# Performance work log

Hardware: AMD Instinct MI355X
Metric: run time of the kernel (lower is better)

Reference implementation:

```python
import jax, jax.numpy as jnp
import numpy as np

N_NODES = 100000
N_EDGES = 1600000
D = 128  # node_feat_size == edge_hidden_size


def setup_inputs() -> dict:
    key = jax.random.key(0)
    ks = jax.random.split(key, 10)
    s = 1.0 / np.sqrt(D)
    return {
        "node_feats": jax.random.normal(ks[0], (N_NODES, D), jnp.float32),
        "edge_logits": jax.random.normal(ks[1], (N_EDGES, 1), jnp.float32),
        "W_proj": jax.random.normal(ks[2], (D, D), jnp.float32) * s,
        "b_proj": jax.random.normal(ks[3], (D,), jnp.float32) * s,
        "W1": jax.random.normal(ks[4], (2 * D, D), jnp.float32) * s,
        "b1": jax.random.normal(ks[5], (D,), jnp.float32) * s,
        "W2": jax.random.normal(ks[6], (D, D), jnp.float32) * s,
        "b2": jax.random.normal(ks[7], (D,), jnp.float32) * s,
        "src": jax.random.randint(ks[8], (N_EDGES,), 0, N_NODES),
        "dst": jax.random.randint(ks[9], (N_EDGES,), 0, N_NODES),
    }


def reference(node_feats, edge_logits, W_proj, b_proj, W1, b1, W2, b2, src, dst):
    # ---- edge_softmax: softmax of edge_logits grouped by destination node ----
    # [E,1] logits; per-dst max for numerical stability (gradient-free shift)
    m = jax.ops.segment_max(edge_logits, dst, num_segments=N_NODES)  # [N,1]
    m = jnp.where(jnp.isfinite(m), m, 0.0)  # nodes with no in-edges
    e = jnp.exp(edge_logits - jax.lax.stop_gradient(m)[dst])  # [E,1]
    z = jax.ops.segment_sum(e, dst, num_segments=N_NODES)  # [N,1]
    a = e / z[dst]  # [E,1]

    # ---- project_node (dropout is identity at inference) ----
    hv = node_feats @ W_proj + b_proj  # [N,D]

    # ---- src_mul_edge + sum aggregation: c[v] = sum_{(u->v)} a_uv * hv[u] ----
    msg = hv[src] * a  # [E,D]
    c = jax.ops.segment_sum(msg, dst, num_segments=N_NODES)  # [N,D]

    context = jax.nn.elu(c)
    x = jnp.concatenate([context, node_feats], axis=1)  # [N,2D]
    h = jax.nn.relu(x @ W1 + b1)  # Linear -> Dropout(id) -> ReLU
    out = jax.nn.relu(h @ W2 + b2)  # Linear -> Dropout(id), outer ReLU
    return out
```

## Files before the change

### kernel.cpp

```cpp
#include <hip/hip_runtime.h>
#include <hip/hip_bf16.h>

typedef __hip_bfloat16 bf16;
typedef __attribute__((ext_vector_type(8))) __bf16 bf16x8;
typedef __attribute__((ext_vector_type(4))) float floatx4;
typedef __attribute__((ext_vector_type(2))) float floatx2;

#define BUCKET_SHIFT 7
#define BUCKET_NODES 128
#define MAX_NB 1024
#define EPB 2048

__device__ __forceinline__ unsigned short f2b(float f) {
    bf16 h = __float2bfloat16(f);
    unsigned short s;
    __builtin_memcpy(&s, &h, 2);
    return s;
}
__device__ __forceinline__ float b2f(unsigned short u) {
    unsigned int x = ((unsigned int)u) << 16;
    float f;
    __builtin_memcpy(&f, &x, 4);
    return f;
}
__device__ __forceinline__ float load_dual(const void* p, long long i, bool isbf) {
    return isbf ? b2f(((const unsigned short*)p)[i]) : ((const float*)p)[i];
}
__device__ __forceinline__ bf16x8 ldsfrag(const unsigned short* p) {
    union { uint4 u; bf16x8 v; } t;
    t.u = *(const uint4*)p;
    return t.v;
}
__device__ __forceinline__ bf16x8 gfrag_dual(const void* A, int row, int stride, int k0, bool isbf) {
    if (isbf) {
        union { uint4 u; bf16x8 v; } t;
        t.u = *(const uint4*)((const unsigned short*)A + (size_t)row * stride + k0);
        return t.v;
    }
    const float* ap = (const float*)A + (size_t)row * stride + k0;
    float4 v0 = ((const float4*)ap)[0];
    float4 v1 = ((const float4*)ap)[1];
    union { unsigned short s[8]; bf16x8 v; } t;
    t.s[0] = f2b(v0.x); t.s[1] = f2b(v0.y); t.s[2] = f2b(v0.z); t.s[3] = f2b(v0.w);
    t.s[4] = f2b(v1.x); t.s[5] = f2b(v1.y); t.s[6] = f2b(v1.z); t.s[7] = f2b(v1.w);
    return t.v;
}

__global__ __launch_bounds__(64) void detect_kernel(const unsigned int* __restrict__ words,
                                                    int* __restrict__ flag,
                                                    int* __restrict__ bcount) {
    for (int i = threadIdx.x; i < MAX_NB; i += 64) bcount[i] = 0;
    int cnt = 0;
    for (int i = threadIdx.x; i < 4096; i += 64) {
        unsigned int lo = words[i] & 0xFFFFu;
        unsigned int e = (lo >> 7) & 0xFFu;
        if (lo == 0u || (e >= 110u && e <= 135u)) cnt++;
    }
#pragma unroll
    for (int off = 32; off > 0; off >>= 1) cnt += __shfl_down(cnt, off, 64);
    if (threadIdx.x == 0) *flag = (cnt > 2458) ? 1 : 0;
}

__global__ __launch_bounds__(256) void prep_kernel(const void* __restrict__ Wp,
                                                   const void* __restrict__ W1,
                                                   const void* __restrict__ W2,
                                                   unsigned short* __restrict__ Wtp,
                                                   unsigned short* __restrict__ Wt1,
                                                   unsigned short* __restrict__ Wt2,
                                                   const int* __restrict__ flag,
                                                   const int* __restrict__ dst,
                                                   int* __restrict__ bcount, int E) {
    if (blockIdx.x < 256) {
        bool isbf = (*flag != 0);
        int idx = blockIdx.x * 256 + threadIdx.x;
        if (idx < 16384) {
            int n = idx >> 7, k = idx & 127;
            Wtp[idx] = f2b(load_dual(Wp, (long long)k * 128 + n, isbf));
        } else if (idx < 49152) {
            int j = idx - 16384;
            int n = j >> 8, k = j & 255;
            Wt1[j] = f2b(load_dual(W1, (long long)k * 128 + n, isbf));
        } else if (idx < 65536) {
            int j = idx - 49152;
            int n = j >> 7, k = j & 127;
            Wt2[j] = f2b(load_dual(W2, (long long)k * 128 + n, isbf));
        }
    } else {
        __shared__ int lcnt[MAX_NB];
        for (int i = threadIdx.x; i < MAX_NB; i += 256) lcnt[i] = 0;
        __syncthreads();
        int base = (blockIdx.x - 256) * EPB;
#pragma unroll
        for (int j = 0; j < EPB / 256; ++j) {
            int e = base + j * 256 + threadIdx.x;
            if (e < E) atomicAdd(&lcnt[dst[e] >> BUCKET_SHIFT], 1);
        }
        __syncthreads();
        for (int i = threadIdx.x; i < MAX_NB; i += 256)
            if (lcnt[i]) atomicAdd(&bcount[i], lcnt[i]);
    }
}

__global__ __launch_bounds__(256) void bscan_kernel(const int* __restrict__ bcount,
                                                    int* __restrict__ bstart,
                                                    int* __restrict__ bcursor, int NB) {
    int t = threadIdx.x;
    int v[4];
    int sum = 0;
#pragma unroll
    for (int j = 0; j < 4; ++j) {
        int i = t * 4 + j;
        v[j] = (i < NB) ? bcount[i] : 0;
        sum += v[j];
    }
    int lane = t & 63, wave = t >> 6;
    int inc = sum;
#pragma unroll
    for (int off = 1; off < 64; off <<= 1) {
        int x = __shfl_up(inc, off, 64);
        if (lane >= off) inc += x;
    }
    __shared__ int wsum[4];
    if (lane == 63) wsum[wave] = inc;
    __syncthreads();
    int woff = 0;
    for (int w = 0; w < wave; ++w) woff += wsum[w];
    int run = inc - sum + woff;
#pragma unroll
    for (int j = 0; j < 4; ++j) {
        int i = t * 4 + j;
        if (i < NB) { bstart[i] = run; bcursor[i] = run; }
        run += v[j];
    }
}

__global__ __launch_bounds__(256) void bappend_kernel(const int* __restrict__ dst,
                                                      const int* __restrict__ src,
                                                      const void* __restrict__ logits,
                                                      int* __restrict__ bcursor,
                                                      uint2* __restrict__ ebuf,
                                                      const int* __restrict__ flag, int E) {
    __shared__ int lcnt[MAX_NB];
    __shared__ int lbase[MAX_NB];
    for (int i = threadIdx.x; i < MAX_NB; i += 256) lcnt[i] = 0;
    __syncthreads();
    const bool isbf = (*flag != 0);
    int base = blockIdx.x * EPB;
#pragma unroll
    for (int j = 0; j < EPB / 256; ++j) {
        int e = base + j * 256 + threadIdx.x;
        if (e < E) atomicAdd(&lcnt[dst[e] >> BUCKET_SHIFT], 1);
    }
    __syncthreads();
    for (int i = threadIdx.x; i < MAX_NB; i += 256) {
        int c = lcnt[i];
        if (c) { lbase[i] = atomicAdd(&bcursor[i], c); lcnt[i] = 0; }
    }
    __syncthreads();
#pragma unroll
    for (int j = 0; j < EPB / 256; ++j) {
        int e = base + j * 256 + threadIdx.x;
        if (e < E) {
            int d = dst[e];
            int b = d >> BUCKET_SHIFT;
            float w = expf(load_dual(logits, e, isbf));
            int pos = lbase[b] + atomicAdd(&lcnt[b], 1);
            uint2 rec;
            rec.x = (unsigned int)src[e] | ((unsigned int)(d & (BUCKET_NODES - 1)) << 24);
            rec.y = __float_as_uint(w);
            ebuf[pos] = rec;
        }
    }
}

__global__ __launch_bounds__(256) void gemm_bcsr_kernel(const void* __restrict__ A,
                                                        const unsigned short* __restrict__ Wt,
                                                        const void* __restrict__ bias,
                                                        unsigned short* __restrict__ hv,
                                                        const int* __restrict__ flag, int N,
                                                        int gblocks,
                                                        const uint2* __restrict__ ebuf,
                                                        const int* __restrict__ bstart,
                                                        const int* __restrict__ bcount,
                                                        uint2* __restrict__ ebuf2,
                                                        int* __restrict__ row_start,
                                                        int* __restrict__ ncount) {
    __shared__ unsigned short Wl[128 * 136];
    if ((int)blockIdx.x < gblocks) {
        const bool isbf = (*flag != 0);
        const int t = threadIdx.x, wid = t >> 6, lane = t & 63;
        const int m16 = lane & 15, quad = lane >> 4;
        const int row0 = blockIdx.x * 128;
        {
            int r = t >> 1, kh = (t & 1) * 64;
            const uint4* s = (const uint4*)(Wt + (size_t)r * 128 + kh);
            uint4* d = (uint4*)&Wl[r * 136 + kh];
#pragma unroll
            for (int q = 0; q < 8; ++q) d[q] = s[q];
        }
        __syncthreads();

        floatx4 acc[2][8];
#pragma unroll
        for (int i = 0; i < 2; ++i)
#pragma unroll
            for (int j = 0; j < 8; ++j) acc[i][j] = (floatx4){0.f, 0.f, 0.f, 0.f};

        int ra0 = row0 + wid * 32 + m16;      if (ra0 >= N) ra0 = N - 1;
        int ra1 = row0 + wid * 32 + 16 + m16; if (ra1 >= N) ra1 = N - 1;

#pragma unroll
        for (int c = 0; c < 4; ++c) {
            int k0 = c * 32 + quad * 8;
            bf16x8 a0 = gfrag_dual(A, ra0, 128, k0, isbf);
            bf16x8 a1 = gfrag_dual(A, ra1, 128, k0, isbf);
#pragma unroll
            for (int nt = 0; nt < 8; ++nt) {
                bf16x8 b = ldsfrag(&Wl[(nt * 16 + m16) * 136 + k0]);
                acc[0][nt] = __builtin_amdgcn_mfma_f32_16x16x32_bf16(a0, b, acc[0][nt], 0, 0, 0);
                acc[1][nt] = __builtin_amdgcn_mfma_f32_16x16x32_bf16(a1, b, acc[1][nt], 0, 0, 0);
            }
        }

#pragma unroll
        for (int mt = 0; mt < 2; ++mt) {
            int gr0 = row0 + wid * 32 + mt * 16 + quad * 4;
#pragma unroll
            for (int nt = 0; nt < 8; ++nt) {
                int col = nt * 16 + m16;
                float bb = load_dual(bias, col, isbf);
#pragma unroll
                for (int rg = 0; rg < 4; ++rg) {
                    int gr = gr0 + rg;
                    if (gr < N) hv[(size_t)gr * 128 + col] = f2b(acc[mt][nt][rg] + bb);
                }
            }
        }
    } else {
        int* lcnt = (int*)Wl;
        int* lbase = lcnt + BUCKET_NODES;
        const int b = blockIdx.x - gblocks;
        const int s0 = bstart[b];
        const int cnt = bcount[b];
        if (threadIdx.x < BUCKET_NODES) lcnt[threadIdx.x] = 0;
        __syncthreads();
        for (int i = threadIdx.x; i < cnt; i += 256)
            atomicAdd(&lcnt[ebuf[s0 + i].x >> 24], 1);
        __syncthreads();
        if (threadIdx.x < 64) {
            int lane = threadIdx.x;
            int carry = 0;
#pragma unroll
            for (int half = 0; half < 2; ++half) {
                int idx = half * 64 + lane;
                int v = lcnt[idx];
                int inc = v;
#pragma unroll
                for (int off = 1; off < 64; off <<= 1) {
                    int t = __shfl_up(inc, off, 64);
                    if (lane >= off) inc += t;
                }
                lbase[idx] = carry + inc - v;
                carry += __shfl(inc, 63, 64);
            }
        }
        __syncthreads();
        if (threadIdx.x < BUCKET_NODES) {
            int gn = b * BUCKET_NODES + threadIdx.x;
            if (gn < N) {
                row_start[gn] = s0 + lbase[threadIdx.x];
                ncount[gn] = lcnt[threadIdx.x];
            }
        }
        __syncthreads();
        if (threadIdx.x < BUCKET_NODES) lcnt[threadIdx.x] = 0;
        __syncthreads();
        for (int i = threadIdx.x; i < cnt; i += 256) {
            uint2 rec = ebuf[s0 + i];
            int dl = rec.x >> 24;
            int pos = lbase[dl] + atomicAdd(&lcnt[dl], 1);
            ebuf2[s0 + pos] = make_uint2(rec.x & 0xFFFFFFu, rec.y);
        }
    }
}

__global__ __launch_bounds__(256) void agg_csr_kernel(const int* __restrict__ row_start,
                                                      const int* __restrict__ ncount,
                                                      const unsigned long long* __restrict__ erec,
                                                      const unsigned int* __restrict__ hv32,
                                                      unsigned int* __restrict__ ctx32, int N) {
    int n = blockIdx.x * 4 + (threadIdx.x >> 6);
    int lane = threadIdx.x & 63;
    if (n >= N) return;
    int s0 = __builtin_amdgcn_readfirstlane(row_start[n]);
    int deg = __builtin_amdgcn_readfirstlane(ncount[n]);
    const unsigned long long* ep = erec + s0;
    const unsigned int lb = (unsigned int)lane << 2;
    floatx2 acc = {0.f, 0.f};
    float z = 0.f;
    int i = 0;
    for (; i + 16 <= deg; i += 16) {
        unsigned long long r[16];
        unsigned int h[16];
#pragma unroll
        for (int j = 0; j < 16; ++j) r[j] = ep[i + j];
#pragma unroll
        for (int j = 0; j < 16; ++j) {
            unsigned int sx = (unsigned int)r[j];
            __builtin_assume(sx < (1u << 24));
            h[j] = *(const unsigned int*)((const char*)hv32 + ((sx << 8) | lb));
        }
#pragma unroll
        for (int j = 0; j < 16; ++j) {
            float w = __uint_as_float((unsigned int)(r[j] >> 32));
            z += w;
            floatx2 hf = { __uint_as_float(h[j] << 16),
                           __uint_as_float(h[j] & 0xFFFF0000u) };
            acc += hf * w;
        }
    }
    for (; i + 4 <= deg; i += 4) {
        unsigned long long r[4];
        unsigned int h[4];
#pragma unroll
        for (int j = 0; j < 4; ++j) r[j] = ep[i + j];
#pragma unroll
        for (int j = 0; j < 4; ++j) {
            unsigned int sx = (unsigned int)r[j];
            __builtin_assume(sx < (1u << 24));
            h[j] = *(const unsigned int*)((const char*)hv32 + ((sx << 8) | lb));
        }
#pragma unroll
        for (int j = 0; j < 4; ++j) {
            float w = __uint_as_float((unsigned int)(r[j] >> 32));
            z += w;
            floatx2 hf = { __uint_as_float(h[j] << 16),
                           __uint_as_float(h[j] & 0xFFFF0000u) };
            acc += hf * w;
        }
    }
    for (; i < deg; ++i) {
        unsigned long long r = ep[i];
        unsigned int sx = (unsigned int)r;
        __builtin_assume(sx < (1u << 24));
        unsigned int h = *(const unsigned int*)((const char*)hv32 + ((sx << 8) | lb));
        float w = __uint_as_float((unsigned int)(r >> 32));
        z += w;
        floatx2 hf = { __uint_as_float(h << 16),
                       __uint_as_float(h & 0xFFFF0000u) };
        acc += hf * w;
    }
    float rz = (z > 0.f) ? 1.f / z : 0.f;
    float x = acc.x * rz, y = acc.y * rz;
    x = x > 0.f ? x : expm1f(x);
    y = y > 0.f ? y : expm1f(y);
    ctx32[(size_t)n * 64 + lane] = ((unsigned int)f2b(y) << 16) | f2b(x);
}

__global__ __launch_bounds__(256) void mlp_fused(const unsigned short* __restrict__ ctx,
                                                 const void* __restrict__ nf,
                                                 const unsigned short* __restrict__ Wt1,
                                                 const void* __restrict__ b1,
                                                 const unsigned short* __restrict__ Wt2,
                                                 const void* __restrict__ b2,
                                                 void* __restrict__ outp,
                                                 const int* __restrict__ flag, int N) {
    __shared__ unsigned short Wl[128 * 72];
    __shared__ unsigned short Hl[4][32 * 136];
    const bool isbf = (*flag != 0);
    const int t = threadIdx.x, wid = t >> 6, lane = t & 63;
    const int m16 = lane & 15, quad = lane >> 4;
    const int row0 = blockIdx.x * 128;

    floatx4 acc[2][8];
#pragma unroll
    for (int i = 0; i < 2; ++i)
#pragma unroll
        for (int j = 0; j < 8; ++j) acc[i][j] = (floatx4){0.f, 0.f, 0.f, 0.f};

    int ra0 = row0 + wid * 32 + m16;      if (ra0 >= N) ra0 = N - 1;
    int ra1 = row0 + wid * 32 + 16 + m16; if (ra1 >= N) ra1 = N - 1;

#pragma unroll
    for (int kc = 0; kc < 4; ++kc) {
        {
            int r = t >> 1, kh = (t & 1) * 32;
            const uint4* s = (const uint4*)(Wt1 + (size_t)r * 256 + kc * 64 + kh);
            uint4* d = (uint4*)&Wl[r * 72 + kh];
#pragma unroll
            for (int q = 0; q < 4; ++q) d[q] = s[q];
        }
        __syncthreads();
#pragma unroll
        for (int c = 0; c < 2; ++c) {
            int kl = c * 32 + quad * 8;
            int ka = kc * 64 + kl;
            bf16x8 a0, a1;
            if (ka < 128) {
                union { uint4 u; bf16x8 v; } t0, t1;
                t0.u = *(const uint4*)(ctx + (size_t)ra0 * 128 + ka);
                t1.u = *(const uint4*)(ctx + (size_t)ra1 * 128 + ka);
                a0 = t0.v; a1 = t1.v;
            } else {
                a0 = gfrag_dual(nf, ra0, 128, ka - 128, isbf);
                a1 = gfrag_dual(nf, ra1, 128, ka - 128, isbf);
            }
#pragma unroll
            for (int nt = 0; nt < 8; ++nt) {
                bf16x8 b = ldsfrag(&Wl[(nt * 16 + m16) * 72 + kl]);
                acc[0][nt] = __builtin_amdgcn_mfma_f32_16x16x32_bf16(a0, b, acc[0][nt], 0, 0, 0);
                acc[1][nt] = __builtin_amdgcn_mfma_f32_16x16x32_bf16(a1, b, acc[1][nt], 0, 0, 0);
            }
        }
        __syncthreads();
    }

#pragma unroll
    for (int nt = 0; nt < 8; ++nt) {
        int col = nt * 16 + m16;
        float bb = load_dual(b1, col, isbf);
#pragma unroll
        for (int mt = 0; mt < 2; ++mt) {
#pragma unroll
            for (int rg = 0; rg < 4; ++rg) {
                int lr = mt * 16 + quad * 4 + rg;
                float x = acc[mt][nt][rg] + bb;
                Hl[wid][lr * 136 + col] = f2b(x > 0.f ? x : 0.f);
            }
        }
    }

#pragma unroll
    for (int i = 0; i < 2; ++i)
#pragma unroll
        for (int j = 0; j < 8; ++j) acc[i][j] = (floatx4){0.f, 0.f, 0.f, 0.f};

#pragma unroll
    for (int kc = 0; kc < 2; ++kc) {
        {
            int r = t >> 1, kh = (t & 1) * 32;
            const uint4* s = (const uint4*)(Wt2 + (size_t)r * 128 + kc * 64 + kh);
            uint4* d = (uint4*)&Wl[r * 72 + kh];
#pragma unroll
            for (int q = 0; q < 4; ++q) d[q] = s[q];
        }
        __syncthreads();
#pragma unroll
        for (int c = 0; c < 2; ++c) {
            int kl = c * 32 + quad * 8;
            int ka = kc * 64 + kl;
            bf16x8 a0 = ldsfrag(&Hl[wid][m16 * 136 + ka]);
            bf16x8 a1 = ldsfrag(&Hl[wid][(16 + m16) * 136 + ka]);
#pragma unroll
            for (int nt = 0; nt < 8; ++nt) {
                bf16x8 b = ldsfrag(&Wl[(nt * 16 + m16) * 72 + kl]);
                acc[0][nt] = __builtin_amdgcn_mfma_f32_16x16x32_bf16(a0, b, acc[0][nt], 0, 0, 0);
                acc[1][nt] = __builtin_amdgcn_mfma_f32_16x16x32_bf16(a1, b, acc[1][nt], 0, 0, 0);
            }
        }
        __syncthreads();
    }

#pragma unroll
    for (int mt = 0; mt < 2; ++mt) {
        int gr0 = row0 + wid * 32 + mt * 16 + quad * 4;
#pragma unroll
        for (int nt = 0; nt < 8; ++nt) {
            int col = nt * 16 + m16;
            float bb = load_dual(b2, col, isbf);
#pragma unroll
            for (int rg = 0; rg < 4; ++rg) {
                int gr = gr0 + rg;
                if (gr < N) {
                    float x = acc[mt][nt][rg] + bb;
                    x = x > 0.f ? x : 0.f;
                    if (!isbf) ((float*)outp)[(size_t)gr * 128 + col] = x;
                    else       ((unsigned short*)outp)[(size_t)gr * 128 + col] = f2b(x);
                }
            }
        }
    }
}

extern "C" void kernel_launch(void* const* d_in, const int* in_sizes, int n_in,
                              void* d_out, int out_size, void* d_ws, size_t ws_size,
                              hipStream_t stream) {
    const void* node_feats  = d_in[0];
    const void* edge_logits = d_in[1];
    const void* W_proj      = d_in[2];
    const void* b_proj      = d_in[3];
    const void* W1          = d_in[4];
    const void* b1          = d_in[5];
    const void* W2          = d_in[6];
    const void* b2          = d_in[7];
    const int*  src         = (const int*)d_in[8];
    const int*  dst         = (const int*)d_in[9];

    const int N = in_sizes[0] / 128;
    const int E = in_sizes[8];
    const int NB = (N + BUCKET_NODES - 1) / BUCKET_NODES;

    char* ws = (char*)d_ws;
    size_t off = 0;
    unsigned short* hv  = (unsigned short*)(ws + off); off += (size_t)N * 256;
    unsigned short* ctx = (unsigned short*)(ws + off); off += (size_t)N * 256;
    uint2* ebuf  = (uint2*)(ws + off); off += (size_t)E * 8;
    uint2* ebuf2 = (uint2*)(ws + off); off += (size_t)E * 8;
    unsigned short* Wtp = (unsigned short*)(ws + off); off += 128 * 128 * 2;
    unsigned short* Wt1 = (unsigned short*)(ws + off); off += 128 * 256 * 2;
    unsigned short* Wt2 = (unsigned short*)(ws + off); off += 128 * 128 * 2;
    int* bcount    = (int*)(ws + off); off += MAX_NB * 4;
    int* bstart    = (int*)(ws + off); off += MAX_NB * 4;
    int* bcursor   = (int*)(ws + off); off += MAX_NB * 4;
    int* row_start = (int*)(ws + off); off += (size_t)N * 4;
    int* ncount    = (int*)(ws + off); off += (size_t)N * 4;
    int* flag      = (int*)(ws + off);

    const int gblocks = (N + 127) / 128;
    const int ebblocks = (E + EPB - 1) / EPB;

    detect_kernel<<<1, 64, 0, stream>>>((const unsigned int*)node_feats, flag, bcount);
    prep_kernel<<<256 + ebblocks, 256, 0, stream>>>(W_proj, W1, W2, Wtp, Wt1, Wt2,
                                                    flag, dst, bcount, E);
    bscan_kernel<<<1, 256, 0, stream>>>(bcount, bstart, bcursor, NB);
    bappend_kernel<<<ebblocks, 256, 0, stream>>>(dst, src, edge_logits, bcursor,
                                                 ebuf, flag, E);
    gemm_bcsr_kernel<<<gblocks + NB, 256, 0, stream>>>(node_feats, Wtp, b_proj, hv,
                                                       flag, N, gblocks,
                                                       ebuf, bstart, bcount, ebuf2,
                                                       row_start, ncount);
    agg_csr_kernel<<<(N + 3) / 4, 256, 0, stream>>>(row_start, ncount,
                                                    (const unsigned long long*)ebuf2,
                                                    (const unsigned int*)hv,
                                                    (unsigned int*)ctx, N);
    mlp_fused<<<gblocks, 256, 0, stream>>>(ctx, node_feats, Wt1, b1, Wt2, b2,
                                           d_out, flag, N);
}
```

Baseline: 344.6 us.

## Fuse bucket counting and append into one segment-local sort pass

Replaces the separate count and append passes over the edges with a single kernel. Each block of 2048 edges bucket-sorts its edges locally in shared memory, writes them back contiguously in its own segment, and records per-bucket offsets for that segment. The later bucket kernel then gathers each bucket's slices from every segment into shared memory before the per-node sort. This removes one full pass over dst, src and logits plus the global cursor atomics. In exchange the gather is serialized per thread with uneven slice sizes, and a bucket holding more than 4352 edges is silently truncated, which assumes a fairly uniform dst distribution.

After: 352.0 us. 2.1% more time.

```diff
diff --git a/kernel.cpp b/kernel.cpp
--- a/kernel.cpp
+++ b/kernel.cpp
@@ -61,18 +61,30 @@
     if (threadIdx.x == 0) *flag = (cnt > 2458) ? 1 : 0;
 }
 
-__global__ __launch_bounds__(256) void prep_kernel(const void* __restrict__ Wp,
-                                                   const void* __restrict__ W1,
-                                                   const void* __restrict__ W2,
-                                                   unsigned short* __restrict__ Wtp,
-                                                   unsigned short* __restrict__ Wt1,
-                                                   unsigned short* __restrict__ Wt2,
-                                                   const int* __restrict__ flag,
-                                                   const int* __restrict__ dst,
-                                                   int* __restrict__ bcount, int E) {
-    if (blockIdx.x < 256) {
-        bool isbf = (*flag != 0);
-        int idx = blockIdx.x * 256 + threadIdx.x;
+__global__ __launch_bounds__(256) void sortseg_kernel(const int* __restrict__ dst,
+                                                      const int* __restrict__ src,
+                                                      const void* __restrict__ logits,
+                                                      uint2* __restrict__ ebuf,
+                                                      int* __restrict__ offs,
+                                                      int* __restrict__ bcount,
+                                                      const void* __restrict__ Wp,
+                                                      const void* __restrict__ W1,
+                                                      const void* __restrict__ W2,
+                                                      unsigned short* __restrict__ Wtp,
+                                                      unsigned short* __restrict__ Wt1,
+                                                      unsigned short* __restrict__ Wt2,
+                                                      const int* __restrict__ flag,
+                                                      int E, int NSEG, int NB) {
+    __shared__ int dstbuf[EPB];
+    __shared__ int lcnt[MAX_NB];
+    __shared__ int loff[MAX_NB + 1];
+    __shared__ uint2 recstage[EPB];
+    __shared__ int wsum[4];
+    const int t = threadIdx.x;
+    const bool isbf = (*flag != 0);
+
+    if ((int)blockIdx.x >= NSEG) {
+        int idx = ((int)blockIdx.x - NSEG) * 256 + t;
         if (idx < 16384) {
             int n = idx >> 7, k = idx & 127;
             Wtp[idx] = f2b(load_dual(Wp, (long long)k * 128 + n, isbf));
@@ -85,25 +97,72 @@
             int n = j >> 7, k = j & 127;
             Wt2[j] = f2b(load_dual(W2, (long long)k * 128 + n, isbf));
         }
-    } else {
-        __shared__ int lcnt[MAX_NB];
-        for (int i = threadIdx.x; i < MAX_NB; i += 256) lcnt[i] = 0;
-        __syncthreads();
-        int base = (blockIdx.x - 256) * EPB;
-#pragma unroll
-        for (int j = 0; j < EPB / 256; ++j) {
-            int e = base + j * 256 + threadIdx.x;
-            if (e < E) atomicAdd(&lcnt[dst[e] >> BUCKET_SHIFT], 1);
-        }
-        __syncthreads();
-        for (int i = threadIdx.x; i < MAX_NB; i += 256)
-            if (lcnt[i]) atomicAdd(&bcount[i], lcnt[i]);
-    }
+        return;
+    }
+
+    const int seg = blockIdx.x;
+    const int base = seg * EPB;
+    for (int i = t; i < MAX_NB; i += 256) lcnt[i] = 0;
+    __syncthreads();
+#pragma unroll
+    for (int j = 0; j < EPB / 256; ++j) {
+        int e = base + j * 256 + t;
+        int d = (e < E) ? dst[e] : -1;
+        dstbuf[j * 256 + t] = d;
+        if (e < E) atomicAdd(&lcnt[d >> BUCKET_SHIFT], 1);
+    }
+    __syncthreads();
+    {
+        int v[4];
+        int sum = 0;
+#pragma unroll
+        for (int j = 0; j < 4; ++j) { v[j] = lcnt[t * 4 + j]; sum += v[j]; }
+        int lane = t & 63, wave = t >> 6;
+        int inc = sum;
+#pragma unroll
+        for (int off = 1; off < 64; off <<= 1) {
+            int x = __shfl_up(inc, off, 64);
+            if (lane >= off) inc += x;
+        }
+        if (lane == 63) wsum[wave] = inc;
+        __syncthreads();
+        int woff = 0;
+        for (int w = 0; w < wave; ++w) woff += wsum[w];
+        int run = inc - sum + woff;
+#pragma unroll
+        for (int j = 0; j < 4; ++j) {
+            int i = t * 4 + j;
+            loff[i] = run;
+            if (v[j]) atomicAdd(&bcount[i], v[j]);
+            lcnt[i] = 0;
+            run += v[j];
+        }
+        if (t == 255) loff[MAX_NB] = run;
+    }
+    __syncthreads();
+#pragma unroll
+    for (int j = 0; j < EPB / 256; ++j) {
+        int e = base + j * 256 + t;
+        if (e < E) {
+            int d = dstbuf[j * 256 + t];
+            int b = d >> BUCKET_SHIFT;
+            float w = expf(load_dual(logits, e, isbf));
+            int pos = loff[b] + atomicAdd(&lcnt[b], 1);
+            recstage[pos] = make_uint2(
+                (unsigned int)src[e] | ((unsigned int)(d & (BUCKET_NODES - 1)) << 24),
+                __float_as_uint(w));
+        }
+    }
+    __syncthreads();
+    const int cnt_seg = loff[MAX_NB];
+    for (int k = t; k < cnt_seg; k += 256)
+        ebuf[base + k] = recstage[k];
+    for (int i = t; i <= NB; i += 256)
+        offs[(size_t)seg * (NB + 1) + i] = loff[i];
 }
 
 __global__ __launch_bounds__(256) void bscan_kernel(const int* __restrict__ bcount,
-                                                    int* __restrict__ bstart,
-                                                    int* __restrict__ bcursor, int NB) {
+                                                    int* __restrict__ bstart, int NB) {
     int t = threadIdx.x;
     int v[4];
     int sum = 0;
@@ -129,47 +188,8 @@
 #pragma unroll
     for (int j = 0; j < 4; ++j) {
         int i = t * 4 + j;
-        if (i < NB) { bstart[i] = run; bcursor[i] = run; }
+        if (i < NB) bstart[i] = run;
         run += v[j];
-    }
-}
-
-__global__ __launch_bounds__(256) void bappend_kernel(const int* __restrict__ dst,
-                                                      const int* __restrict__ src,
-                                                      const void* __restrict__ logits,
-                                                      int* __restrict__ bcursor,
-                                                      uint2* __restrict__ ebuf,
-                                                      const int* __restrict__ flag, int E) {
-    __shared__ int lcnt[MAX_NB];
-    __shared__ int lbase[MAX_NB];
-    for (int i = threadIdx.x; i < MAX_NB; i += 256) lcnt[i] = 0;
-    __syncthreads();
-    const bool isbf = (*flag != 0);
-    int base = blockIdx.x * EPB;
-#pragma unroll
-    for (int j = 0; j < EPB / 256; ++j) {
-        int e = base + j * 256 + threadIdx.x;
-        if (e < E) atomicAdd(&lcnt[dst[e] >> BUCKET_SHIFT], 1);
-    }
-    __syncthreads();
-    for (int i = threadIdx.x; i < MAX_NB; i += 256) {
-        int c = lcnt[i];
-        if (c) { lbase[i] = atomicAdd(&bcursor[i], c); lcnt[i] = 0; }
-    }
-    __syncthreads();
-#pragma unroll
-    for (int j = 0; j < EPB / 256; ++j) {
-        int e = base + j * 256 + threadIdx.x;
-        if (e < E) {
-            int d = dst[e];
-            int b = d >> BUCKET_SHIFT;
-            float w = expf(load_dual(logits, e, isbf));
-            int pos = lbase[b] + atomicAdd(&lcnt[b], 1);
-            uint2 rec;
-            rec.x = (unsigned int)src[e] | ((unsigned int)(d & (BUCKET_NODES - 1)) << 24);
-            rec.y = __float_as_uint(w);
-            ebuf[pos] = rec;
-        }
     }
 }
 
@@ -181,11 +201,15 @@
                                                         int gblocks,
                                                         const uint2* __restrict__ ebuf,
                                                         const int* __restrict__ bstart,
-                                                        const int* __restrict__ bcount,
+                                                        const int* __restrict__ offs,
                                                         uint2* __restrict__ ebuf2,
                                                         int* __restrict__ row_start,
-                                                        int* __restrict__ ncount) {
+                                                        int* __restrict__ ncount,
+                                                        int NSEG, int NB) {
     __shared__ unsigned short Wl[128 * 136];
+    __shared__ int lcnt2[BUCKET_NODES];
+    __shared__ int lbase2[BUCKET_NODES];
+    __shared__ int bwsum[4];
     if ((int)blockIdx.x < gblocks) {
         const bool isbf = (*flag != 0);
         const int t = threadIdx.x, wid = t >> 6, lane = t & 63;
@@ -237,48 +261,77 @@
             }
         }
     } else {
-        int* lcnt = (int*)Wl;
-        int* lbase = lcnt + BUCKET_NODES;
-        const int b = blockIdx.x - gblocks;
+        uint2* buf = (uint2*)Wl;
+        const int b = (int)blockIdx.x - gblocks;
+        const int t = threadIdx.x;
         const int s0 = bstart[b];
-        const int cnt = bcount[b];
-        if (threadIdx.x < BUCKET_NODES) lcnt[threadIdx.x] = 0;
-        __syncthreads();
-        for (int i = threadIdx.x; i < cnt; i += 256)
-            atomicAdd(&lcnt[ebuf[s0 + i].x >> 24], 1);
-        __syncthreads();
-        if (threadIdx.x < 64) {
-            int lane = threadIdx.x;
+        int sgi[8], sgc[8];
+        int nmy = 0, mycnt = 0;
+        for (int s = t; s < NSEG && nmy < 8; s += 256) {
+            int st = offs[(size_t)s * (NB + 1) + b];
+            int en = offs[(size_t)s * (NB + 1) + b + 1];
+            sgi[nmy] = s * EPB + st;
+            sgc[nmy] = en - st;
+            mycnt += en - st;
+            ++nmy;
+        }
+        int lane = t & 63, wave = t >> 6;
+        int inc = mycnt;
+#pragma unroll
+        for (int off = 1; off < 64; off <<= 1) {
+            int x = __shfl_up(inc, off, 64);
+            if (lane >= off) inc += x;
+        }
+        if (lane == 63) bwsum[wave] = inc;
+        __syncthreads();
+        int woff = 0;
+        for (int w = 0; w < wave; ++w) woff += bwsum[w];
+        const int total = bwsum[0] + bwsum[1] + bwsum[2] + bwsum[3];
+        int p = woff + inc - mycnt;
+        for (int k = 0; k < nmy; ++k) {
+            int g = sgi[k];
+            for (int i = 0; i < sgc[k]; ++i) {
+                if (p < 4352) buf[p] = ebuf[g + i];
+                ++p;
+            }
+        }
+        __syncthreads();
+        if (t < BUCKET_NODES) lcnt2[t] = 0;
+        __syncthreads();
+        for (int i = t; i < total; i += 256)
+            atomicAdd(&lcnt2[buf[i].x >> 24], 1);
+        __syncthreads();
+        if (t < 64) {
             int carry = 0;
 #pragma unroll
             for (int half = 0; half < 2; ++half) {
-                int idx = half * 64 + lane;
-                int v = lcnt[idx];
-                int inc = v;
+                int idx = half * 64 + t;
+                int v = lcnt2[idx];
+                int inc2 = v;
 #pragma unroll
                 for (int off = 1; off < 64; off <<= 1) {
-                    int t = __shfl_up(inc, off, 64);
-                    if (lane >= off) inc += t;
+                    int x = __shfl_up(inc2, off, 64);
+                    if (t >= off) inc2 += x;
                 }
-                lbase[idx] = carry + inc - v;
-                carry += __shfl(inc, 63, 64);
-            }
-        }
-        __syncthreads();
-        if (threadIdx.x < BUCKET_NODES) {
-            int gn = b * BUCKET_NODES + threadIdx.x;
+                lbase2[idx] = carry + inc2 - v;
+                carry += __shfl(inc2, 63, 64);
+            }
+        }
+        __syncthreads();
+        if (t < BUCKET_NODES) {
+            int gn = b * BUCKET_NODES + t;
             if (gn < N) {
-                row_start[gn] = s0 + lbase[threadIdx.x];
-                ncount[gn] = lcnt[threadIdx.x];
-            }
-        }
-        __syncthreads();
-        if (threadIdx.x < BUCKET_NODES) lcnt[threadIdx.x] = 0;
-        __syncthreads();
-        for (int i = threadIdx.x; i < cnt; i += 256) {
-            uint2 rec = ebuf[s0 + i];
+                row_start[gn] = s0 + lbase2[t];
+                ncount[gn] = lcnt2[t];
+            }
+        }
+        __syncthreads();
+        if (t < BUCKET_NODES) lcnt2[t] = 0;
+        __syncthreads();
+        for (int i = t; i < total; i += 256) {
+            uint2 rec = buf[i];
             int dl = rec.x >> 24;
-            int pos = lbase[dl] + atomicAdd(&lcnt[dl], 1);
+            int pos = lbase2[dl] + atomicAdd(&lcnt2[dl], 1);
             ebuf2[s0 + pos] = make_uint2(rec.x & 0xFFFFFFu, rec.y);
         }
     }
@@ -499,6 +552,7 @@
     const int N = in_sizes[0] / 128;
     const int E = in_sizes[8];
     const int NB = (N + BUCKET_NODES - 1) / BUCKET_NODES;
+    const int NSEG = (E + EPB - 1) / EPB;
 
     char* ws = (char*)d_ws;
     size_t off = 0;
@@ -511,24 +565,22 @@
     unsigned short* Wt2 = (unsigned short*)(ws + off); off += 128 * 128 * 2;
     int* bcount    = (int*)(ws + off); off += MAX_NB * 4;
     int* bstart    = (int*)(ws + off); off += MAX_NB * 4;
-    int* bcursor   = (int*)(ws + off); off += MAX_NB * 4;
+    int* offs      = (int*)(ws + off); off += (size_t)NSEG * (NB + 1) * 4;
     int* row_start = (int*)(ws + off); off += (size_t)N * 4;
     int* ncount    = (int*)(ws + off); off += (size_t)N * 4;
     int* flag      = (int*)(ws + off);
 
     const int gblocks = (N + 127) / 128;
-    const int ebblocks = (E + EPB - 1) / EPB;
 
     detect_kernel<<<1, 64, 0, stream>>>((const unsigned int*)node_feats, flag, bcount);
-    prep_kernel<<<256 + ebblocks, 256, 0, stream>>>(W_proj, W1, W2, Wtp, Wt1, Wt2,
-                                                    flag, dst, bcount, E);
-    bscan_kernel<<<1, 256, 0, stream>>>(bcount, bstart, bcursor, NB);
-    bappend_kernel<<<ebblocks, 256, 0, stream>>>(dst, src, edge_logits, bcursor,
-                                                 ebuf, flag, E);
+    sortseg_kernel<<<NSEG + 256, 256, 0, stream>>>(dst, src, edge_logits, ebuf, offs,
+                                                   bcount, W_proj, W1, W2,
+                                                   Wtp, Wt1, Wt2, flag, E, NSEG, NB);
+    bscan_kernel<<<1, 256, 0, stream>>>(bcount, bstart, NB);
     gemm_bcsr_kernel<<<gblocks + NB, 256, 0, stream>>>(node_feats, Wtp, b_proj, hv,
                                                        flag, N, gblocks,
-                                                       ebuf, bstart, bcount, ebuf2,
-                                                       row_start, ncount);
+                                                       ebuf, bstart, offs, ebuf2,
+                                                       row_start, ncount, NSEG, NB);
     agg_csr_kernel<<<(N + 3) / 4, 256, 0, stream>>>(row_start, ncount,
                                                     (const unsigned long long*)ebuf2,
                                                     (const unsigned int*)hv,
```
